# Kernel optimization log

Hardware: AMD Instinct MI355X
Metric: run time of the kernel (lower is better)

The kernel has to match this reference:

```python
import jax, jax.numpy as jnp
import numpy as np

H = 32      # num attention heads
HD = 64     # head dim
RD = 16     # rotary dim = 0.25 * head_dim (partial rotary)
EPS = 1e-5
BASE = 10000.0


def _ln(x, w, b):
    m = x.mean(-1, keepdims=True)
    v = ((x - m) ** 2).mean(-1, keepdims=True)
    return (x - m) / jnp.sqrt(v + EPS) * w + b


def _rot_half(x):
    x1, x2 = jnp.split(x, 2, axis=-1)
    return jnp.concatenate([-x2, x1], axis=-1)


def setup_inputs() -> dict:
    key = jax.random.key(0)
    ks = jax.random.split(key, 16)
    B, S, D, FF = 1, 2048, 2048, 8192
    std = 0.02
    hidden_states = jax.random.normal(ks[0], (B, S, D), jnp.float32)
    memory = jax.random.normal(ks[1], (B, S, D), jnp.float32)
    # causal additive mask (B,1,S,S): 0 where allowed, -inf above diagonal
    causal = jnp.where(jnp.tril(jnp.ones((S, S), bool)), 0.0, -jnp.inf).astype(jnp.float32)
    attention_mask = jnp.broadcast_to(causal[None, None], (B, 1, S, S))
    position_ids = jnp.broadcast_to(jnp.arange(S, dtype=jnp.int32), (B, S))
    return {
        'hidden_states': hidden_states,
        'memory': memory,
        'attention_mask': attention_mask,
        'position_ids': position_ids,
        'ln1_w': jnp.ones((D,), jnp.float32),
        'ln1_b': jnp.zeros((D,), jnp.float32),
        'ln2_w': jnp.ones((D,), jnp.float32),
        'ln2_b': jnp.zeros((D,), jnp.float32),
        'Wq': jax.random.normal(ks[2], (D, D), jnp.float32) * std,
        'Wk': jax.random.normal(ks[3], (D, D), jnp.float32) * std,
        'Wv': jax.random.normal(ks[4], (D, D), jnp.float32) * std,
        'Wo': jax.random.normal(ks[5], (D, D), jnp.float32) * std,
        'Wg': jax.random.normal(ks[6], (FF, D), jnp.float32) * std,
        'Wu': jax.random.normal(ks[7], (FF, D), jnp.float32) * std,
        'Wd': jax.random.normal(ks[8], (D, FF), jnp.float32) * std,
    }


def reference(hidden_states, memory, attention_mask, position_ids,
              ln1_w, ln1_b, ln2_w, ln2_b, Wq, Wk, Wv, Wo, Wg, Wu, Wd):
    B, S, D = hidden_states.shape
    residual = hidden_states
    h = _ln(hidden_states, ln1_w, ln1_b)
    mem = _ln(memory, ln1_w, ln1_b)

    # fast_forward: concat memory in front along sequence
    x = jnp.concatenate([mem, h], axis=1)              # (B, 2S, D)
    pos = jnp.concatenate([position_ids, position_ids], axis=1)  # (B, 2S)
    L = 2 * S

    q = (x @ Wq.T).reshape(B, L, H, HD).transpose(0, 2, 1, 3)  # (B,H,2S,HD)
    k = (x @ Wk.T).reshape(B, L, H, HD).transpose(0, 2, 1, 3)
    v = (x @ Wv.T).reshape(B, L, H, HD).transpose(0, 2, 1, 3)

    # partial rotary embedding
    inv_freq = 1.0 / (BASE ** (jnp.arange(0, RD, 2, dtype=jnp.float32) / RD))
    t = pos.astype(jnp.float32)[:, :, None] * inv_freq       # (B,2S,RD/2)
    emb = jnp.concatenate([t, t], axis=-1)                   # (B,2S,RD)
    cos = jnp.cos(emb)[:, None]                              # (B,1,2S,RD)
    sin = jnp.sin(emb)[:, None]
    qr, qp = q[..., :RD], q[..., RD:]
    kr, kp = k[..., :RD], k[..., RD:]
    qr = qr * cos + _rot_half(qr) * sin
    kr = kr * cos + _rot_half(kr) * sin
    q = jnp.concatenate([qr, qp], axis=-1)
    k = jnp.concatenate([kr, kp], axis=-1)

    # only non-memory queries attend
    q = q[:, :, S:]                                          # (B,H,S,HD)
    scores = jnp.einsum('bhqd,bhkd->bhqk', q, k) / jnp.sqrt(jnp.float32(HD))  # (B,H,S,2S)

    # left mask: causal + no attending to own memory slot; right: only own position (+ causal)
    eye = jnp.eye(S, dtype=bool)[None, None]
    left = jnp.where(eye, -jnp.inf, attention_mask)
    right = jnp.where(eye, attention_mask, -jnp.inf)
    mask = jnp.concatenate([left, right], axis=-1)           # (B,1,S,2S)

    w = jax.nn.softmax((scores + mask).astype(jnp.float32), axis=-1).astype(q.dtype)
    attn = jnp.einsum('bhqk,bhkd->bhqd', w, v)
    attn = attn.transpose(0, 2, 1, 3).reshape(B, S, D) @ Wo.T

    h = residual + attn
    residual2 = h
    h2 = _ln(h, ln2_w, ln2_b)
    mlp = (jax.nn.silu(h2 @ Wg.T) * (h2 @ Wu.T)) @ Wd.T
    return residual2 + mlp
```

## Files before the change

### kernel.cpp

```cpp
#include <hip/hip_runtime.h>
#include <stdint.h>
#include <stddef.h>

typedef short s16;
typedef __attribute__((ext_vector_type(8))) short short8;
typedef __attribute__((ext_vector_type(4))) float float4v;

#define S_LEN 2048
#define DMODEL 2048
#define LLEN 4096
#define FFDIM 8192
#define NHEAD 32
#define HDIM 64

#define AS1 __attribute__((address_space(1)))
#define AS3 __attribute__((address_space(3)))

__device__ __forceinline__ float bf2f(short s) {
  union { uint32_t u; float f; } x;
  x.u = ((uint32_t)(uint16_t)s) << 16;
  return x.f;
}
__device__ __forceinline__ short f2bf(float f) {
  union { float f; uint32_t u; } x;
  x.f = f;
  uint32_t r = x.u + 0x7fffu + ((x.u >> 16) & 1u);
  return (short)(r >> 16);
}

template <typename T> __device__ __forceinline__ float ldv(const T* p, size_t i);
template <> __device__ __forceinline__ float ldv<float>(const float* p, size_t i) { return p[i]; }
template <> __device__ __forceinline__ float ldv<s16>(const s16* p, size_t i) { return bf2f(p[i]); }
template <typename T> __device__ __forceinline__ void stv(T* p, size_t i, float v);
template <> __device__ __forceinline__ void stv<float>(float* p, size_t i, float v) { p[i] = v; }
template <> __device__ __forceinline__ void stv<s16>(s16* p, size_t i, float v) { p[i] = f2bf(v); }

__global__ __launch_bounds__(256) void w2bf(const float* __restrict__ src, s16* __restrict__ dst,
                                            int n8) {
  const int i = blockIdx.x * 256 + threadIdx.x;
  if (i >= n8) return;
  const float4v a = ((const float4v*)src)[2 * i];
  const float4v b = ((const float4v*)src)[2 * i + 1];
  short8 o;
#pragma unroll
  for (int j = 0; j < 4; j++) { o[j] = f2bf(a[j]); o[j + 4] = f2bf(b[j]); }
  ((short8*)dst)[i] = o;
}

template <typename T>
__global__ __launch_bounds__(256) void ln_kernel(const T* __restrict__ src,
                                                 const float* __restrict__ w,
                                                 const float* __restrict__ b,
                                                 s16* __restrict__ dst) {
  const int row = blockIdx.x, t = threadIdx.x;
  float v[8];
  float s = 0.f, s2 = 0.f;
#pragma unroll
  for (int i = 0; i < 8; i++) {
    v[i] = ldv<T>(src, (size_t)row * DMODEL + t * 8 + i);
    s += v[i];
    s2 += v[i] * v[i];
  }
#pragma unroll
  for (int off = 32; off > 0; off >>= 1) {
    s += __shfl_down(s, off);
    s2 += __shfl_down(s2, off);
  }
  __shared__ float rs[4], rs2[4];
  if ((t & 63) == 0) { rs[t >> 6] = s; rs2[t >> 6] = s2; }
  __syncthreads();
  const float fs = rs[0] + rs[1] + rs[2] + rs[3];
  const float fs2 = rs2[0] + rs2[1] + rs2[2] + rs2[3];
  const float mean = fs * (1.f / (float)DMODEL);
  const float var = fs2 * (1.f / (float)DMODEL) - mean * mean;
  const float rstd = rsqrtf(var + 1e-5f);
  const float4v w0 = *(const float4v*)(w + t * 8);
  const float4v w1 = *(const float4v*)(w + t * 8 + 4);
  const float4v b0 = *(const float4v*)(b + t * 8);
  const float4v b1 = *(const float4v*)(b + t * 8 + 4);
  short8 o;
#pragma unroll
  for (int i = 0; i < 4; i++) {
    o[i] = f2bf((v[i] - mean) * rstd * w0[i] + b0[i]);
    o[i + 4] = f2bf((v[i + 4] - mean) * rstd * w1[i] + b1[i]);
  }
  *(short8*)(dst + (size_t)row * DMODEL + t * 8) = o;
}

__global__ __launch_bounds__(256) void init_out(float4v* __restrict__ dst,
                                                const float4v* __restrict__ src, int n4) {
  const int i = blockIdx.x * 256 + threadIdx.x;
  if (i < n4) dst[i] = src ? src[i] : float4v{0.f, 0.f, 0.f, 0.f};
}

template <typename T>
__global__ __launch_bounds__(256) void rope_kernel(T* __restrict__ buf, const int* __restrict__ pos,
                                                   int nrows) {
  const int idx = blockIdx.x * 256 + threadIdx.x;
  if (idx >= nrows * NHEAD) return;
  const int row = idx >> 5, h = idx & 31;
  const int pid = pos[row < S_LEN ? row : row - S_LEN];
  T* ptr = buf + (size_t)row * DMODEL + h * HDIM;
  float a[8], c[8];
  if constexpr (sizeof(T) == 2) {
    const short8 r0 = *(const short8*)ptr;
    const short8 r1 = *(const short8*)(ptr + 8);
#pragma unroll
    for (int f = 0; f < 8; f++) { a[f] = bf2f(r0[f]); c[f] = bf2f(r1[f]); }
  } else {
    const float4v x0 = *(const float4v*)ptr;
    const float4v x1 = *(const float4v*)(ptr + 4);
    const float4v x2 = *(const float4v*)(ptr + 8);
    const float4v x3 = *(const float4v*)(ptr + 12);
#pragma unroll
    for (int f = 0; f < 4; f++) { a[f] = x0[f]; a[f + 4] = x1[f]; c[f] = x2[f]; c[f + 4] = x3[f]; }
  }
  const float inv_freq[8] = {1.0f, 0.31622776601683794f, 0.1f, 0.031622776601683794f,
                             0.01f, 0.0031622776601683794f, 0.001f, 0.00031622776601683794f};
  const float fp = (float)pid;
  float o0[8], o1[8];
#pragma unroll
  for (int f = 0; f < 8; f++) {
    float sv, cv;
    sincosf(fp * inv_freq[f], &sv, &cv);
    o0[f] = a[f] * cv - c[f] * sv;
    o1[f] = c[f] * cv + a[f] * sv;
  }
  if constexpr (sizeof(T) == 2) {
    short8 w0, w1;
#pragma unroll
    for (int f = 0; f < 8; f++) { w0[f] = f2bf(o0[f]); w1[f] = f2bf(o1[f]); }
    *(short8*)ptr = w0;
    *(short8*)(ptr + 8) = w1;
  } else {
    float4v y0, y1, y2, y3;
#pragma unroll
    for (int f = 0; f < 4; f++) { y0[f] = o0[f]; y1[f] = o0[f + 4]; y2[f] = o1[f]; y3[f] = o1[f + 4]; }
    *(float4v*)ptr = y0;
    *(float4v*)(ptr + 4) = y1;
    *(float4v*)(ptr + 8) = y2;
    *(float4v*)(ptr + 12) = y3;
  }
}

template <int EPI, int BSRC, typename AUXT, typename OUTT>
__global__ __launch_bounds__(256) void gemm_bt(const s16* __restrict__ A, const void* __restrict__ Wp,
                                               OUTT* __restrict__ C, const AUXT* __restrict__ aux,
                                               int M, int N, int K) {
  __shared__ alignas(16) s16 As[128 * 32];
  __shared__ alignas(16) s16 Bs[128 * 32];
  const int t = threadIdx.x;
  const int wave = t >> 6, lane = t & 63;
  const int quad = lane >> 4, l15 = lane & 15;
  const int n0 = blockIdx.x * 128, m0 = blockIdx.y * 128;
  const int wm = wave >> 1, wn = wave & 1;
  const int srow = lane >> 2, skk = (lane & 3) * 8;
  const int br4 = t >> 2, bc4 = (t & 3) * 8;
  const int kchunk = K / (int)gridDim.z;
  const int kbeg = kchunk * (int)blockIdx.z;

  float4v acc[4][4];
#pragma unroll
  for (int i = 0; i < 4; i++)
#pragma unroll
    for (int j = 0; j < 4; j++) acc[i][j] = float4v{0.f, 0.f, 0.f, 0.f};

  const float* wrow0 = (const float*)Wp + (size_t)(n0 + br4) * K + bc4;
  const float* wrow1 = wrow0 + (size_t)64 * K;
  const s16* Wb = (const s16*)Wp;

  for (int k0 = kbeg; k0 < kbeg + kchunk; k0 += 32) {
    if constexpr (BSRC == 0) {
      float4v wa0 = *(const float4v*)(wrow0 + k0);
      float4v wa1 = *(const float4v*)(wrow0 + k0 + 4);
      float4v wb0 = *(const float4v*)(wrow1 + k0);
      float4v wb1 = *(const float4v*)(wrow1 + k0 + 4);
      __syncthreads();
#pragma unroll
      for (int cc = 0; cc < 2; cc++) {
        const int ci = wave * 2 + cc;
        const s16* ga = A + (size_t)(m0 + ci * 16 + srow) * K + (k0 + skk);
        __builtin_amdgcn_global_load_lds((const AS1 void*)ga, (AS3 void*)(&As[ci * 512]), 16, 0, 0);
      }
      short8 c0, c1;
#pragma unroll
      for (int i = 0; i < 4; i++) {
        c0[i] = f2bf(wa0[i]);
        c0[i + 4] = f2bf(wa1[i]);
        c1[i] = f2bf(wb0[i]);
        c1[i + 4] = f2bf(wb1[i]);
      }
      *(short8*)&Bs[br4 * 32 + bc4] = c0;
      *(short8*)&Bs[(64 + br4) * 32 + bc4] = c1;
    } else {
      __syncthreads();
#pragma unroll
      for (int cc = 0; cc < 2; cc++) {
        const int ci = wave * 2 + cc;
        const s16* ga = A + (size_t)(m0 + ci * 16 + srow) * K + (k0 + skk);
        __builtin_amdgcn_global_load_lds((const AS1 void*)ga, (AS3 void*)(&As[ci * 512]), 16, 0, 0);
        const s16* gb = Wb + (size_t)(n0 + ci * 16 + srow) * K + (k0 + skk);
        __builtin_amdgcn_global_load_lds((const AS1 void*)gb, (AS3 void*)(&Bs[ci * 512]), 16, 0, 0);
      }
    }
    __syncthreads();
    short8 a[4], b[4];
#pragma unroll
    for (int mt = 0; mt < 4; mt++)
      a[mt] = *(const short8*)&As[(wm * 64 + mt * 16 + l15) * 32 + quad * 8];
#pragma unroll
    for (int nt = 0; nt < 4; nt++)
      b[nt] = *(const short8*)&Bs[(wn * 64 + nt * 16 + l15) * 32 + quad * 8];
#pragma unroll
    for (int mt = 0; mt < 4; mt++)
#pragma unroll
      for (int nt = 0; nt < 4; nt++)
        acc[mt][nt] = __builtin_amdgcn_mfma_f32_16x16x32_bf16(a[mt], b[nt], acc[mt][nt], 0, 0, 0);
  }
#pragma unroll
  for (int mt = 0; mt < 4; mt++) {
#pragma unroll
    for (int nt = 0; nt < 4; nt++) {
      const float* av = (const float*)&acc[mt][nt];
      const int col = n0 + wn * 64 + nt * 16 + l15;
      const int rowb = m0 + wm * 64 + mt * 16 + quad * 4;
#pragma unroll
      for (int r = 0; r < 4; r++) {
        const size_t idx = (size_t)(rowb + r) * N + col;
        float v = av[r];
        if constexpr (EPI == 3) {
          unsafeAtomicAdd((float*)&C[idx], v);
        } else {
          if (EPI == 1) v += ldv<AUXT>(aux, idx);
          if (EPI == 2) { const float g = ldv<AUXT>(aux, idx); v *= g / (1.0f + __expf(-g)); }
          stv<OUTT>(C, idx, v);
        }
      }
    }
  }
}

__global__ __launch_bounds__(256) void attn_kernel(const float* __restrict__ qb, const s16* __restrict__ kb,
                                                   const s16* __restrict__ vb, s16* __restrict__ attn) {
  __shared__ alignas(16) s16 Qs[64 * 72];
  __shared__ alignas(16) s16 Ks[64 * 72];
  __shared__ alignas(16) s16 Vt[64 * 72];
  __shared__ alignas(16) s16 Ps[64 * 72];
  const int t = threadIdx.x;
  const int h = blockIdx.x & 31;
  const int qblk = 31 - (int)(blockIdx.x >> 5);
  const int wave = t >> 6, lane = t & 63;
  const int quad = lane >> 4, l15 = lane & 15;

#pragma unroll
  for (int rr = 0; rr < 2; rr++) {
    const int tt = t + rr * 256;
    const int i = tt >> 3, d0 = (tt & 7) * 8;
    const float* qp = qb + (size_t)(qblk * 64 + i) * DMODEL + h * HDIM + d0;
    const float4v q0 = *(const float4v*)qp;
    const float4v q1 = *(const float4v*)(qp + 4);
    short8 o;
#pragma unroll
    for (int x = 0; x < 4; x++) { o[x] = f2bf(q0[x]); o[x + 4] = f2bf(q1[x]); }
    *(short8*)&Qs[i * 72 + d0] = o;
  }

  float4v O[4];
#pragma unroll
  for (int i = 0; i < 4; i++) O[i] = float4v{0.f, 0.f, 0.f, 0.f};
  float m_run[4] = {-1e30f, -1e30f, -1e30f, -1e30f};
  float l_run[4] = {0.f, 0.f, 0.f, 0.f};

  const float SCALE = 0.125f * 1.442695040888963f;

  const int j0 = t >> 3, d00 = (t & 7) * 8;
  const int vkeyw = (d00 >> 3) & 7;
  const size_t colb = (size_t)h * HDIM + d00;

  const int nchunks = qblk + 2;
  short8 kr0 = *(const short8*)(kb + (size_t)j0 * DMODEL + colb);
  short8 kr1 = *(const short8*)(kb + (size_t)(j0 + 32) * DMODEL + colb);
  short8 vr0 = *(const short8*)(vb + (size_t)j0 * DMODEL + colb);
  short8 vr1 = *(const short8*)(vb + (size_t)(j0 + 32) * DMODEL + colb);

  for (int c = 0; c < nchunks; ++c) {
    asm volatile("s_waitcnt lgkmcnt(0)" ::: "memory");
    __builtin_amdgcn_s_barrier();
    asm volatile("" ::: "memory");
    *(short8*)&Ks[j0 * 72 + d00] = kr0;
    *(short8*)&Ks[(j0 + 32) * 72 + d00] = kr1;
#pragma unroll
    for (int x = 0; x < 8; x++) {
      Vt[(d00 + x) * 72 + (j0 ^ (vkeyw << 3))] = vr0[x];
      Vt[(d00 + x) * 72 + ((j0 + 32) ^ (vkeyw << 3))] = vr1[x];
    }
    if (c + 1 < nchunks) {
      const int krow = (c + 1 <= qblk) ? (c + 1) * 64 : (S_LEN + qblk * 64);
      kr0 = *(const short8*)(kb + (size_t)(krow + j0) * DMODEL + colb);
      kr1 = *(const short8*)(kb + (size_t)(krow + j0 + 32) * DMODEL + colb);
      vr0 = *(const short8*)(vb + (size_t)(krow + j0) * DMODEL + colb);
      vr1 = *(const short8*)(vb + (size_t)(krow + j0 + 32) * DMODEL + colb);
    }
    asm volatile("s_waitcnt lgkmcnt(0)" ::: "memory");
    __builtin_amdgcn_s_barrier();
    asm volatile("" ::: "memory");

    float4v Sacc[4];
#pragma unroll
    for (int i = 0; i < 4; i++) Sacc[i] = float4v{0.f, 0.f, 0.f, 0.f};
    __builtin_amdgcn_s_setprio(1);
#pragma unroll
    for (int ks = 0; ks < 2; ks++) {
      const short8 af = *(const short8*)&Qs[(wave * 16 + l15) * 72 + ks * 32 + quad * 8];
#pragma unroll
      for (int nt = 0; nt < 4; nt++) {
        const short8 bf = *(const short8*)&Ks[(nt * 16 + l15) * 72 + ks * 32 + quad * 8];
        Sacc[nt] = __builtin_amdgcn_mfma_f32_16x16x32_bf16(af, bf, Sacc[nt], 0, 0, 0);
      }
    }
    __builtin_amdgcn_s_setprio(0);
    float* sp = (float*)Sacc;
    if (c < qblk) {
#pragma unroll
      for (int i = 0; i < 16; i++) sp[i] = fminf(sp[i] * SCALE, 2e4f);
    } else {
#pragma unroll
      for (int nt = 0; nt < 4; nt++)
#pragma unroll
        for (int r = 0; r < 4; r++) {
          const int il = wave * 16 + quad * 4 + r;
          const int jl = nt * 16 + l15;
          const bool ok = (c == qblk) ? (jl < il) : (jl == il);
          sp[nt * 4 + r] = ok ? fminf(sp[nt * 4 + r] * SCALE, 2e4f) : -1e30f;
        }
    }
#pragma unroll
    for (int r = 0; r < 4; r++) {
      float mx = fmaxf(fmaxf(sp[0 * 4 + r], sp[1 * 4 + r]), fmaxf(sp[2 * 4 + r], sp[3 * 4 + r]));
#pragma unroll
      for (int off = 1; off < 16; off <<= 1) mx = fmaxf(mx, __shfl_xor(mx, off));
      const float mnew = fmaxf(m_run[r], mx);
      float alpha, sum;
      if (mnew < -1e29f) {
        alpha = 1.f; sum = 0.f;
#pragma unroll
        for (int nt = 0; nt < 4; nt++) sp[nt * 4 + r] = 0.f;
      } else {
        alpha = exp2f(m_run[r] - mnew);
        m_run[r] = mnew;
        sum = 0.f;
#pragma unroll
        for (int nt = 0; nt < 4; nt++) {
          const float p = exp2f(sp[nt * 4 + r] - mnew);
          sp[nt * 4 + r] = p;
          sum += p;
        }
      }
#pragma unroll
      for (int off = 1; off < 16; off <<= 1) sum += __shfl_xor(sum, off);
      l_run[r] = l_run[r] * alpha + sum;
      float* op = (float*)O;
#pragma unroll
      for (int dt = 0; dt < 4; dt++) op[dt * 4 + r] *= alpha;
    }
#pragma unroll
    for (int nt = 0; nt < 4; nt++)
#pragma unroll
      for (int r = 0; r < 4; r++)
        Ps[(wave * 16 + quad * 4 + r) * 72 + nt * 16 + l15] = f2bf(sp[nt * 4 + r]);
    __builtin_amdgcn_s_setprio(1);
#pragma unroll
    for (int ks = 0; ks < 2; ks++) {
      const short8 pf = *(const short8*)&Ps[(wave * 16 + l15) * 72 + ks * 32 + quad * 8];
#pragma unroll
      for (int dt = 0; dt < 4; dt++) {
        const int dd = dt * 16 + l15;
        const int vkey = (dd >> 3) & 7;
        const short8 vf = *(const short8*)&Vt[dd * 72 + ((ks * 32 + quad * 8) ^ (vkey << 3))];
        O[dt] = __builtin_amdgcn_mfma_f32_16x16x32_bf16(pf, vf, O[dt], 0, 0, 0);
      }
    }
    __builtin_amdgcn_s_setprio(0);
  }
  const float* op = (const float*)O;
#pragma unroll
  for (int dt = 0; dt < 4; dt++)
#pragma unroll
    for (int r = 0; r < 4; r++) {
      const int row = qblk * 64 + wave * 16 + quad * 4 + r;
      const int col = h * HDIM + dt * 16 + l15;
      const float inv_l = 1.0f / fmaxf(l_run[r], 1e-20f);
      attn[(size_t)row * DMODEL + col] = f2bf(op[dt * 4 + r] * inv_l);
    }
}

extern "C" void kernel_launch(void* const* d_in, const int* in_sizes, int n_in,
                              void* d_out, int out_size, void* d_ws, size_t ws_size,
                              hipStream_t stream) {
  const float* hidden = (const float*)d_in[0];
  const float* memory = (const float*)d_in[1];
  const int* pos_ids = (const int*)d_in[3];
  const float* ln1_w = (const float*)d_in[4];
  const float* ln1_b = (const float*)d_in[5];
  const float* ln2_w = (const float*)d_in[6];
  const float* ln2_b = (const float*)d_in[7];
  const float* Wq = (const float*)d_in[8];
  const float* Wk = (const float*)d_in[9];
  const float* Wv = (const float*)d_in[10];
  const float* Wo = (const float*)d_in[11];
  const float* Wg = (const float*)d_in[12];
  const float* Wu = (const float*)d_in[13];
  const float* Wd = (const float*)d_in[14];
  s16* ws = (s16*)d_ws;
  const size_t M1 = (size_t)1024 * 1024;

  s16* x = ws;
  float* q = (float*)d_out;
  s16* k = ws + 8 * M1;
  s16* v = ws + 16 * M1;
  s16* attn = ws;
  s16* h2 = ws + 4 * M1;
  s16* g = ws + 8 * M1;

  const bool bw = ws_size >= (size_t)88 * M1 * sizeof(s16);
  s16* Wqb = ws + 24 * M1;
  s16* Wkb = Wqb + 4 * M1;
  s16* Wvb = Wkb + 4 * M1;
  s16* Wob = Wvb + 4 * M1;
  s16* Wgb = Wob + 4 * M1;
  s16* Wub = Wgb + 16 * M1;
  s16* Wdb = Wub + 16 * M1;

  if (bw) {
    w2bf<<<2048, 256, 0, stream>>>(Wq, Wqb, 512 * 1024);
    w2bf<<<2048, 256, 0, stream>>>(Wk, Wkb, 512 * 1024);
    w2bf<<<2048, 256, 0, stream>>>(Wv, Wvb, 512 * 1024);
    w2bf<<<2048, 256, 0, stream>>>(Wo, Wob, 512 * 1024);
    w2bf<<<8192, 256, 0, stream>>>(Wg, Wgb, 2048 * 1024);
    w2bf<<<8192, 256, 0, stream>>>(Wu, Wub, 2048 * 1024);
    w2bf<<<8192, 256, 0, stream>>>(Wd, Wdb, 2048 * 1024);
  }

  ln_kernel<float><<<S_LEN, 256, 0, stream>>>(memory, ln1_w, ln1_b, x);
  ln_kernel<float><<<S_LEN, 256, 0, stream>>>(hidden, ln1_w, ln1_b, x + (size_t)S_LEN * DMODEL);
  init_out<<<4096, 256, 0, stream>>>((float4v*)d_out, (const float4v*)nullptr, 1 << 20);
  if (bw) {
    gemm_bt<3, 1, float, float><<<dim3(16, 16, 4), 256, 0, stream>>>(x + (size_t)S_LEN * DMODEL, Wqb, q, (const float*)nullptr, S_LEN, DMODEL, DMODEL);
    gemm_bt<0, 1, s16, s16><<<dim3(16, 32), 256, 0, stream>>>(x, Wkb, k, (const s16*)nullptr, LLEN, DMODEL, DMODEL);
    gemm_bt<0, 1, s16, s16><<<dim3(16, 32), 256, 0, stream>>>(x, Wvb, v, (const s16*)nullptr, LLEN, DMODEL, DMODEL);
  } else {
    gemm_bt<3, 0, float, float><<<dim3(16, 16, 4), 256, 0, stream>>>(x + (size_t)S_LEN * DMODEL, Wq, q, (const float*)nullptr, S_LEN, DMODEL, DMODEL);
    gemm_bt<0, 0, s16, s16><<<dim3(16, 32), 256, 0, stream>>>(x, Wk, k, (const s16*)nullptr, LLEN, DMODEL, DMODEL);
    gemm_bt<0, 0, s16, s16><<<dim3(16, 32), 256, 0, stream>>>(x, Wv, v, (const s16*)nullptr, LLEN, DMODEL, DMODEL);
  }
  rope_kernel<float><<<(S_LEN * NHEAD) / 256, 256, 0, stream>>>(q, pos_ids, S_LEN);
  rope_kernel<s16><<<(LLEN * NHEAD) / 256, 256, 0, stream>>>(k, pos_ids, LLEN);
  attn_kernel<<<NHEAD * (S_LEN / 64), 256, 0, stream>>>(q, k, v, attn);
  init_out<<<4096, 256, 0, stream>>>((float4v*)d_out, (const float4v*)hidden, 1 << 20);
  if (bw)
    gemm_bt<3, 1, float, float><<<dim3(16, 16, 4), 256, 0, stream>>>(attn, Wob, (float*)d_out, (const float*)nullptr, S_LEN, DMODEL, DMODEL);
  else
    gemm_bt<3, 0, float, float><<<dim3(16, 16, 4), 256, 0, stream>>>(attn, Wo, (float*)d_out, (const float*)nullptr, S_LEN, DMODEL, DMODEL);
  ln_kernel<float><<<S_LEN, 256, 0, stream>>>((const float*)d_out, ln2_w, ln2_b, h2);
  if (bw) {
    gemm_bt<0, 1, s16, s16><<<dim3(64, 16), 256, 0, stream>>>(h2, Wgb, g, (const s16*)nullptr, S_LEN, FFDIM, DMODEL);
    gemm_bt<2, 1, s16, s16><<<dim3(64, 16), 256, 0, stream>>>(h2, Wub, g, g, S_LEN, FFDIM, DMODEL);
    gemm_bt<3, 1, float, float><<<dim3(16, 16, 4), 256, 0, stream>>>(g, Wdb, (float*)d_out, (const float*)nullptr, S_LEN, DMODEL, FFDIM);
  } else {
    gemm_bt<0, 0, s16, s16><<<dim3(64, 16), 256, 0, stream>>>(h2, Wg, g, (const s16*)nullptr, S_LEN, FFDIM, DMODEL);
    gemm_bt<2, 0, s16, s16><<<dim3(64, 16), 256, 0, stream>>>(h2, Wu, g, g, S_LEN, FFDIM, DMODEL);
    gemm_bt<3, 0, float, float><<<dim3(16, 16, 4), 256, 0, stream>>>(g, Wd, (float*)d_out, (const float*)nullptr, S_LEN, DMODEL, FFDIM);
  }
}
```

Before: 1.015 ms.

## Triple-buffer LDS with async prefetch in bf16-weight GEMM path

For the GEMM path whose B operand is already bf16, the shared tiles become three buffers. Global-to-LDS loads are issued two k-steps ahead and gated with manual vmcnt waits plus a single barrier per step, so memory latency overlaps with MFMA work. The fp32-weight path keeps its old single-buffer loop. This triples LDS use per block (48KB), which may lower occupancy, and it relies on exact vmcnt accounting to stay correct.

Result: faster. 942.5 us (-7.2%).

```diff
diff --git a/kernel.cpp b/kernel.cpp
--- a/kernel.cpp
+++ b/kernel.cpp
@@ -147,8 +147,8 @@
 __global__ __launch_bounds__(256) void gemm_bt(const s16* __restrict__ A, const void* __restrict__ Wp,
                                                OUTT* __restrict__ C, const AUXT* __restrict__ aux,
                                                int M, int N, int K) {
-  __shared__ alignas(16) s16 As[128 * 32];
-  __shared__ alignas(16) s16 Bs[128 * 32];
+  __shared__ alignas(16) s16 As[3][128 * 32];
+  __shared__ alignas(16) s16 Bs[3][128 * 32];
   const int t = threadIdx.x;
   const int wave = t >> 6, lane = t & 63;
   const int quad = lane >> 4, l15 = lane & 15;
@@ -165,12 +165,59 @@
 #pragma unroll
     for (int j = 0; j < 4; j++) acc[i][j] = float4v{0.f, 0.f, 0.f, 0.f};
 
-  const float* wrow0 = (const float*)Wp + (size_t)(n0 + br4) * K + bc4;
-  const float* wrow1 = wrow0 + (size_t)64 * K;
   const s16* Wb = (const s16*)Wp;
 
-  for (int k0 = kbeg; k0 < kbeg + kchunk; k0 += 32) {
-    if constexpr (BSRC == 0) {
+  if constexpr (BSRC == 1) {
+    const int nsteps = kchunk >> 5;
+    auto stage = [&](int buf, int k0) {
+#pragma unroll
+      for (int cc = 0; cc < 2; cc++) {
+        const int ci = wave * 2 + cc;
+        const s16* ga = A + (size_t)(m0 + ci * 16 + srow) * K + (k0 + skk);
+        __builtin_amdgcn_global_load_lds((const AS1 void*)ga, (AS3 void*)(&As[buf][ci * 512]), 16, 0, 0);
+        const s16* gb = Wb + (size_t)(n0 + ci * 16 + srow) * K + (k0 + skk);
+        __builtin_amdgcn_global_load_lds((const AS1 void*)gb, (AS3 void*)(&Bs[buf][ci * 512]), 16, 0, 0);
+      }
+    };
+    stage(0, kbeg);
+    if (nsteps > 1) {
+      stage(1, kbeg + 32);
+      asm volatile("s_waitcnt vmcnt(4)" ::: "memory");
+    } else {
+      asm volatile("s_waitcnt vmcnt(0)" ::: "memory");
+    }
+    __builtin_amdgcn_s_barrier();
+    asm volatile("" ::: "memory");
+    int cur = 0;
+    for (int s = 0; s < nsteps; ++s) {
+      short8 a[4], b[4];
+#pragma unroll
+      for (int mt = 0; mt < 4; mt++)
+        a[mt] = *(const short8*)&As[cur][(wm * 64 + mt * 16 + l15) * 32 + quad * 8];
+#pragma unroll
+      for (int nt = 0; nt < 4; nt++)
+        b[nt] = *(const short8*)&Bs[cur][(wn * 64 + nt * 16 + l15) * 32 + quad * 8];
+      if (s + 2 < nsteps) {
+        int nb = cur + 2; if (nb >= 3) nb -= 3;
+        stage(nb, kbeg + (s + 2) * 32);
+      }
+#pragma unroll
+      for (int mt = 0; mt < 4; mt++)
+#pragma unroll
+        for (int nt = 0; nt < 4; nt++)
+          acc[mt][nt] = __builtin_amdgcn_mfma_f32_16x16x32_bf16(a[mt], b[nt], acc[mt][nt], 0, 0, 0);
+      if (s + 1 < nsteps) {
+        if (s + 2 < nsteps) asm volatile("s_waitcnt vmcnt(4)" ::: "memory");
+        else asm volatile("s_waitcnt vmcnt(0)" ::: "memory");
+        __builtin_amdgcn_s_barrier();
+        asm volatile("" ::: "memory");
+      }
+      cur = (cur == 2) ? 0 : cur + 1;
+    }
+  } else {
+    const float* wrow0 = (const float*)Wp + (size_t)(n0 + br4) * K + bc4;
+    const float* wrow1 = wrow0 + (size_t)64 * K;
+    for (int k0 = kbeg; k0 < kbeg + kchunk; k0 += 32) {
       float4v wa0 = *(const float4v*)(wrow0 + k0);
       float4v wa1 = *(const float4v*)(wrow0 + k0 + 4);
       float4v wb0 = *(const float4v*)(wrow1 + k0);
@@ -180,7 +227,7 @@
       for (int cc = 0; cc < 2; cc++) {
         const int ci = wave * 2 + cc;
         const s16* ga = A + (size_t)(m0 + ci * 16 + srow) * K + (k0 + skk);
-        __builtin_amdgcn_global_load_lds((const AS1 void*)ga, (AS3 void*)(&As[ci * 512]), 16, 0, 0);
+        __builtin_amdgcn_global_load_lds((const AS1 void*)ga, (AS3 void*)(&As[0][ci * 512]), 16, 0, 0);
       }
       short8 c0, c1;
 #pragma unroll
@@ -190,32 +237,22 @@
         c1[i] = f2bf(wb0[i]);
         c1[i + 4] = f2bf(wb1[i]);
       }
-      *(short8*)&Bs[br4 * 32 + bc4] = c0;
-      *(short8*)&Bs[(64 + br4) * 32 + bc4] = c1;
-    } else {
+      *(short8*)&Bs[0][br4 * 32 + bc4] = c0;
+      *(short8*)&Bs[0][(64 + br4) * 32 + bc4] = c1;
       __syncthreads();
-#pragma unroll
-      for (int cc = 0; cc < 2; cc++) {
-        const int ci = wave * 2 + cc;
-        const s16* ga = A + (size_t)(m0 + ci * 16 + srow) * K + (k0 + skk);
-        __builtin_amdgcn_global_load_lds((const AS1 void*)ga, (AS3 void*)(&As[ci * 512]), 16, 0, 0);
-        const s16* gb = Wb + (size_t)(n0 + ci * 16 + srow) * K + (k0 + skk);
-        __builtin_amdgcn_global_load_lds((const AS1 void*)gb, (AS3 void*)(&Bs[ci * 512]), 16, 0, 0);
-      }
-    }
-    __syncthreads();
-    short8 a[4], b[4];
-#pragma unroll
-    for (int mt = 0; mt < 4; mt++)
-      a[mt] = *(const short8*)&As[(wm * 64 + mt * 16 + l15) * 32 + quad * 8];
-#pragma unroll
-    for (int nt = 0; nt < 4; nt++)
-      b[nt] = *(const short8*)&Bs[(wn * 64 + nt * 16 + l15) * 32 + quad * 8];
-#pragma unroll
-    for (int mt = 0; mt < 4; mt++)
+      short8 a[4], b[4];
+#pragma unroll
+      for (int mt = 0; mt < 4; mt++)
+        a[mt] = *(const short8*)&As[0][(wm * 64 + mt * 16 + l15) * 32 + quad * 8];
 #pragma unroll
       for (int nt = 0; nt < 4; nt++)
-        acc[mt][nt] = __builtin_amdgcn_mfma_f32_16x16x32_bf16(a[mt], b[nt], acc[mt][nt], 0, 0, 0);
+        b[nt] = *(const short8*)&Bs[0][(wn * 64 + nt * 16 + l15) * 32 + quad * 8];
+#pragma unroll
+      for (int mt = 0; mt < 4; mt++)
+#pragma unroll
+        for (int nt = 0; nt < 4; nt++)
+          acc[mt][nt] = __builtin_amdgcn_mfma_f32_16x16x32_bf16(a[mt], b[nt], acc[mt][nt], 0, 0, 0);
+    }
   }
 #pragma unroll
   for (int mt = 0; mt < 4; mt++) {
```
